# Kernel tuning notes

Hardware: AMD Instinct MI355X
Metric: run time of the kernel (lower is better)

The kernel has to match this reference:

```python
import jax, jax.numpy as jnp
import numpy as np

TAU = 0.5

def setup_inputs() -> dict:
    key = jax.random.key(0)
    kx, ky = jax.random.split(key)
    B, H = 8192, 256
    x = jax.random.normal(kx, (B, H), dtype=jnp.float32)
    y = jax.random.normal(ky, (B, H), dtype=jnp.float32)
    return {"x": x, "y": y}

def reference(x, y):
    # L2-normalize rows
    x_norm = x / jnp.linalg.norm(x, axis=1, keepdims=True)
    y_norm = y / jnp.linalg.norm(y, axis=1, keepdims=True)
    xy_norm = jnp.concatenate([x_norm, y_norm], axis=0)  # [2N, H]
    yx_norm = jnp.concatenate([y_norm, x_norm], axis=0)  # [2N, H]
    # [2N, 2N] cosine-similarity matrix (dominant memory traffic)
    sim_mat_1 = xy_norm @ xy_norm.T
    exp_mat = jnp.exp(sim_mat_1 / TAU)
    exp_row_sum = jnp.sum(exp_mat, axis=1)
    exp_diag = jnp.diagonal(exp_mat)
    denominator = exp_row_sum - exp_diag
    # diag(xy_norm @ yx_norm.T) is the row-wise dot product (avoids redundant NxN matmul)
    pos_sim = jnp.sum(xy_norm * yx_norm, axis=1)
    numerator = jnp.exp(pos_sim / TAU)
    nt_xent = -jnp.log(numerator / denominator)
    return jnp.mean(nt_xent)
```

## Files before the change

### kernel.cpp

```cpp
#include <hip/hip_runtime.h>
#include <hip/hip_bf16.h>
#include <hip/hip_fp8.h>
#include <math.h>

constexpr int NROWS = 8192;
constexpr int HDIM  = 256;
constexpr int N2    = 16384;
constexpr int BM    = 128;
constexpr int NTILE = N2 / BM;
constexpr int NBLK  = NTILE * (NTILE + 1) / 2;

constexpr float ZSCALE    = 16.0f;
constexpr float ACC2EXP2  = 2.885390082f / 256.0f;

typedef __attribute__((ext_vector_type(4))) float floatx4;

#define DPP_ADD(v, CTRL) do {                                                \
    union { float f; int i; } _u, _r; _u.f = (v);                            \
    _r.i = __builtin_amdgcn_update_dpp(0, _u.i, (CTRL), 0xF, 0xF, true);     \
    (v) += _r.f; } while (0)
#define DPP_ROW_SUM16(v) do { DPP_ADD(v,0x101); DPP_ADD(v,0x102);            \
    DPP_ADD(v,0x104); DPP_ADD(v,0x108); } while (0)
#define DPP_ALL_SUM16(v) do { DPP_ADD(v,0xB1); DPP_ADD(v,0x4E);              \
    DPP_ADD(v,0x124); DPP_ADD(v,0x128); } while (0)


__global__ __launch_bounds__(256) void normalize_kernel(
    const float* __restrict__ x, const float* __restrict__ y,
    unsigned char* __restrict__ Zp8, float* __restrict__ pos,
    float* __restrict__ rowsum, float* __restrict__ out)
{
    const int wave = threadIdx.x >> 6, lane = threadIdx.x & 63;
    const int row  = blockIdx.x * 4 + wave;

    const float4 xv = ((const float4*)x)[row * 64 + lane];
    const float4 yv = ((const float4*)y)[row * 64 + lane];

    float sx  = xv.x*xv.x + xv.y*xv.y + xv.z*xv.z + xv.w*xv.w;
    float sy  = yv.x*yv.x + yv.y*yv.y + yv.z*yv.z + yv.w*yv.w;
    float sxy = xv.x*yv.x + xv.y*yv.y + xv.z*yv.z + xv.w*yv.w;
    DPP_ALL_SUM16(sx); DPP_ALL_SUM16(sy); DPP_ALL_SUM16(sxy);
    sx  += __shfl_xor(sx, 16);  sx  += __shfl_xor(sx, 32);
    sy  += __shfl_xor(sy, 16);  sy  += __shfl_xor(sy, 32);
    sxy += __shfl_xor(sxy, 16); sxy += __shfl_xor(sxy, 32);

    const float rxn = rsqrtf(sx), ryn = rsqrtf(sy);
    const float rx = rxn * ZSCALE, ry = ryn * ZSCALE;

    auto pack4 = [](float a, float b, float c, float d) -> unsigned int {
        __hip_fp8_e4m3 f0(a), f1(b), f2(c), f3(d);
        return (unsigned int)f0.__x | ((unsigned int)f1.__x << 8) |
               ((unsigned int)f2.__x << 16) | ((unsigned int)f3.__x << 24);
    };
    const unsigned int wx = pack4(xv.x * rx, xv.y * rx, xv.z * rx, xv.w * rx);
    const unsigned int wy = pack4(yv.x * ry, yv.y * ry, yv.z * ry, yv.w * ry);

    const int tile = row >> 4, m = row & 15;
    const size_t off = (size_t)tile * 4096 + (lane >> 1) * 128 + m * 8 + (lane & 1) * 4;
    *(unsigned int*)(Zp8 + off)                         = wx;
    *(unsigned int*)(Zp8 + off + (size_t)512 * 4096)    = wy;

    if (lane == 0) {
        const float p = sxy * rxn * ryn;
        pos[row]         = p;
        pos[row + NROWS] = p;
    }
    const int gt = blockIdx.x * 256 + threadIdx.x;
    if (gt < N2) rowsum[gt] = 0.f;
    if (gt == 0) out[0] = 0.f;
}

__global__ __launch_bounds__(256, 4) void simgemm_kernel(
    const unsigned char* __restrict__ Zp8, float* __restrict__ rowsum)
{
    const int b = blockIdx.x;
    const int k = b & 7;
    const int m = b >> 3;
    int bi, bj;
    if (m < 136) {
        int ti = (int)((33.0f - sqrtf(1089.0f - 8.0f * (float)m)) * 0.5f);
        if (m < ti * (33 - ti) / 2) ti--;
        else if (m >= (ti + 1) * (32 - ti) / 2) ti++;
        const int tj = ti + (m - ti * (33 - ti) / 2);
        bi = k * 16 + ti;
        bj = k * 16 + tj;
    } else {
        const int m2 = m - 136;
        const int hh = m2 >> 7;
        const int r  = m2 & 127;
        const int h  = hh * 8 + k;
        const int q  = h >> 1;
        const int sub = h & 1;
        int gi = 0;
        #pragma unroll
        for (int t = 6; t > 0; --t)
            if (q >= t * (15 - t) / 2) { gi = t; break; }
        const int gj = gi + 1 + (q - gi * (15 - gi) / 2);
        bi = gi * 16 + sub * 8 + (r >> 4);
        bj = gj * 16 + (r & 15);
    }
    const bool diag = (bi == bj);

    __shared__ float rs[BM];
    __shared__ float cs[BM];

    const int tid  = threadIdx.x;
    const int wave = tid >> 6;
    const int lane = tid & 63;
    const int wm   = wave & 1;
    const int wn   = wave >> 1;
    const int g    = lane >> 4;
    const int m15  = lane & 15;

    if (tid < BM) { rs[tid] = 0.f; cs[tid] = 0.f; }
    __syncthreads();

    const unsigned char* pA = Zp8 + (size_t)(bi * 8 + wm * 4) * 4096 + lane * 8;
    const unsigned char* pB = Zp8 + (size_t)(bj * 8 + wn * 4) * 4096 + lane * 8;

    floatx4 acc[4][4] = {};
    long af[3][4], bf[3][4];

    #pragma unroll
    for (int f = 0; f < 4; ++f) {
        af[0][f] = *(const long*)(pA + f * 4096);
        bf[0][f] = *(const long*)(pB + f * 4096);
    }
    #pragma unroll
    for (int f = 0; f < 4; ++f) {
        af[1][f] = *(const long*)(pA + f * 4096 + 512);
        bf[1][f] = *(const long*)(pB + f * 4096 + 512);
    }

    #pragma unroll
    for (int s = 0; s < HDIM / 32; ++s) {
        const int cur = s % 3;
        if (s + 2 < HDIM / 32) {
            const int nxt = (s + 2) % 3;
            #pragma unroll
            for (int f = 0; f < 4; ++f) {
                af[nxt][f] = *(const long*)(pA + f * 4096 + (s + 2) * 512);
                bf[nxt][f] = *(const long*)(pB + f * 4096 + (s + 2) * 512);
            }
        }
        #pragma unroll
        for (int fm = 0; fm < 4; ++fm)
            #pragma unroll
            for (int fn = 0; fn < 4; ++fn)
                acc[fm][fn] = __builtin_amdgcn_mfma_f32_16x16x32_fp8_fp8(
                    af[cur][fm], bf[cur][fn], acc[fm][fn], 0, 0, 0);
    }

    float rp[4][4] = {{0.f}};
    float cp[4]    = {0.f};

    if (!diag) {
        #pragma unroll
        for (int fm = 0; fm < 4; ++fm)
            #pragma unroll
            for (int fn = 0; fn < 4; ++fn) {
                const floatx4 a = acc[fm][fn];
                #pragma unroll
                for (int q = 0; q < 4; ++q) {
                    const float e = __builtin_amdgcn_exp2f(a[q] * ACC2EXP2);
                    rp[fm][q] += e;
                    cp[fn]    += e;
                }
            }
    } else {
        #pragma unroll
        for (int fm = 0; fm < 4; ++fm)
            #pragma unroll
            for (int fn = 0; fn < 4; ++fn) {
                const floatx4 a = acc[fm][fn];
                const int cl = wn * 64 + fn * 16 + m15;
                #pragma unroll
                for (int q = 0; q < 4; ++q) {
                    const int rl = wm * 64 + fm * 16 + g * 4 + q;
                    float e = __builtin_amdgcn_exp2f(a[q] * ACC2EXP2);
                    if (cl <= rl) e = 0.f;
                    rp[fm][q] += e;
                    cp[fn]    += e;
                }
            }
    }

    #pragma unroll
    for (int fm = 0; fm < 4; ++fm)
        #pragma unroll
        for (int q = 0; q < 4; ++q) {
            float v = rp[fm][q];
            DPP_ROW_SUM16(v);
            rp[fm][q] = v;
        }
    if (m15 == 0) {
        #pragma unroll
        for (int fm = 0; fm < 4; ++fm)
            #pragma unroll
            for (int q = 0; q < 4; ++q)
                atomicAdd(&rs[wm * 64 + fm * 16 + g * 4 + q], rp[fm][q]);
    }

    #pragma unroll
    for (int mask = 16; mask < 64; mask <<= 1)
        #pragma unroll
        for (int fn = 0; fn < 4; ++fn)
            cp[fn] += __shfl_xor(cp[fn], mask);
    if (g == 0) {
        #pragma unroll
        for (int fn = 0; fn < 4; ++fn)
            atomicAdd(&cs[wn * 64 + fn * 16 + m15], cp[fn]);
    }

    __syncthreads();
    if (tid < BM) {
        atomicAdd(&rowsum[(size_t)bi * BM + tid], rs[tid]);
        atomicAdd(&rowsum[(size_t)bj * BM + tid], cs[tid]);
    }
}

__global__ __launch_bounds__(1024) void finalize_kernel(
    const float* __restrict__ rowsum, const float* __restrict__ pos,
    float* __restrict__ out)
{
    const int i = threadIdx.x + blockIdx.x * 1024;
    float s = logf(rowsum[i]) - 2.0f * pos[i];
    #pragma unroll
    for (int off = 32; off; off >>= 1) s += __shfl_down(s, off);
    __shared__ float sh[16];
    const int lt = threadIdx.x;
    if ((lt & 63) == 0) sh[lt >> 6] = s;
    __syncthreads();
    if (lt == 0) {
        float tot = 0.f;
        #pragma unroll
        for (int w = 0; w < 16; ++w) tot += sh[w];
        atomicAdd(out, tot / (float)N2);
    }
}

extern "C" void kernel_launch(void* const* d_in, const int* in_sizes, int n_in,
                              void* d_out, int out_size, void* d_ws, size_t ws_size,
                              hipStream_t stream)
{
    const float* x = (const float*)d_in[0];
    const float* y = (const float*)d_in[1];

    unsigned char* Zp8 = (unsigned char*)d_ws;
    float* rowsum = (float*)((char*)d_ws + (size_t)N2 * HDIM);
    float* pos    = rowsum + N2;

    normalize_kernel<<<NROWS / 4, 256, 0, stream>>>(x, y, Zp8, pos, rowsum, (float*)d_out);
    simgemm_kernel<<<NBLK, 256, 0, stream>>>(Zp8, rowsum);
    finalize_kernel<<<N2 / 1024, 1024, 0, stream>>>(rowsum, pos, (float*)d_out);
}
```

Before: 163.3 us.

## Switch to 32x32x16 FP8 MFMA layout and fuse finalize via last-block reduction

Repacks the normalized FP8 matrix into 32-row tiles and replaces the 16x16x32 MFMA with the 32x32x16 variant, reshaping the epilogue reductions for the new accumulator layout. The finalize kernel is removed: each GEMM block bumps a global counter and the last block computes the log-sum loss. The aim is fewer MFMA instructions and operand loads per tile plus one less kernel launch. The cost is a serial tail reduction in a single block and a weaker memory-ordering pattern, since the counter uses relaxed atomics.

New measurement: 194.7 us. 19.2% more time.

```diff
diff --git a/kernel.cpp b/kernel.cpp
--- a/kernel.cpp
+++ b/kernel.cpp
@@ -13,22 +13,23 @@
 constexpr float ZSCALE    = 16.0f;
 constexpr float ACC2EXP2  = 2.885390082f / 256.0f;
 
-typedef __attribute__((ext_vector_type(4))) float floatx4;
+typedef __attribute__((ext_vector_type(16))) float floatx16;
 
 #define DPP_ADD(v, CTRL) do {                                                \
     union { float f; int i; } _u, _r; _u.f = (v);                            \
     _r.i = __builtin_amdgcn_update_dpp(0, _u.i, (CTRL), 0xF, 0xF, true);     \
     (v) += _r.f; } while (0)
-#define DPP_ROW_SUM16(v) do { DPP_ADD(v,0x101); DPP_ADD(v,0x102);            \
-    DPP_ADD(v,0x104); DPP_ADD(v,0x108); } while (0)
 #define DPP_ALL_SUM16(v) do { DPP_ADD(v,0xB1); DPP_ADD(v,0x4E);              \
     DPP_ADD(v,0x124); DPP_ADD(v,0x128); } while (0)
+#define DPP_SUM32_TO_L31(v) do { DPP_ADD(v,0x111); DPP_ADD(v,0x112);         \
+    DPP_ADD(v,0x114); DPP_ADD(v,0x118); DPP_ADD(v,0x142); } while (0)
 
 
 __global__ __launch_bounds__(256) void normalize_kernel(
     const float* __restrict__ x, const float* __restrict__ y,
     unsigned char* __restrict__ Zp8, float* __restrict__ pos,
-    float* __restrict__ rowsum, float* __restrict__ out)
+    float* __restrict__ rowsum, int* __restrict__ counter,
+    float* __restrict__ out)
 {
     const int wave = threadIdx.x >> 6, lane = threadIdx.x & 63;
     const int row  = blockIdx.x * 4 + wave;
@@ -55,10 +56,10 @@
     const unsigned int wx = pack4(xv.x * rx, xv.y * rx, xv.z * rx, xv.w * rx);
     const unsigned int wy = pack4(yv.x * ry, yv.y * ry, yv.z * ry, yv.w * ry);
 
-    const int tile = row >> 4, m = row & 15;
-    const size_t off = (size_t)tile * 4096 + (lane >> 1) * 128 + m * 8 + (lane & 1) * 4;
+    const size_t off = (size_t)(row >> 5) * 8192 + (lane >> 1) * 256
+                     + (row & 31) * 8 + (lane & 1) * 4;
     *(unsigned int*)(Zp8 + off)                         = wx;
-    *(unsigned int*)(Zp8 + off + (size_t)512 * 4096)    = wy;
+    *(unsigned int*)(Zp8 + off + (size_t)256 * 8192)    = wy;
 
     if (lane == 0) {
         const float p = sxy * rxn * ryn;
@@ -67,11 +68,13 @@
     }
     const int gt = blockIdx.x * 256 + threadIdx.x;
     if (gt < N2) rowsum[gt] = 0.f;
-    if (gt == 0) out[0] = 0.f;
+    if (gt == 0) { *counter = 0; out[0] = 0.f; }
 }
 
 __global__ __launch_bounds__(256, 4) void simgemm_kernel(
-    const unsigned char* __restrict__ Zp8, float* __restrict__ rowsum)
+    const unsigned char* __restrict__ Zp8, float* __restrict__ rowsum,
+    const float* __restrict__ pos, int* __restrict__ counter,
+    float* __restrict__ out)
 {
     const int b = blockIdx.x;
     const int k = b & 7;
@@ -103,113 +106,100 @@
 
     __shared__ float rs[BM];
     __shared__ float cs[BM];
+    __shared__ int   isLast;
 
     const int tid  = threadIdx.x;
     const int wave = tid >> 6;
     const int lane = tid & 63;
     const int wm   = wave & 1;
     const int wn   = wave >> 1;
-    const int g    = lane >> 4;
-    const int m15  = lane & 15;
+    const int hl   = lane >> 5;
+    const int c31  = lane & 31;
 
     if (tid < BM) { rs[tid] = 0.f; cs[tid] = 0.f; }
     __syncthreads();
 
-    const unsigned char* pA = Zp8 + (size_t)(bi * 8 + wm * 4) * 4096 + lane * 8;
-    const unsigned char* pB = Zp8 + (size_t)(bj * 8 + wn * 4) * 4096 + lane * 8;
-
-    floatx4 acc[4][4] = {};
+    const unsigned char* pA = Zp8 + (size_t)(bi * 4 + wm * 2) * 8192 + lane * 8;
+    const unsigned char* pB = Zp8 + (size_t)(bj * 4 + wn * 2) * 8192 + lane * 8;
+
+    floatx16 acc[2][2] = {};
     long af[3][4], bf[3][4];
 
-    #pragma unroll
-    for (int f = 0; f < 4; ++f) {
-        af[0][f] = *(const long*)(pA + f * 4096);
-        bf[0][f] = *(const long*)(pB + f * 4096);
-    }
-    #pragma unroll
-    for (int f = 0; f < 4; ++f) {
-        af[1][f] = *(const long*)(pA + f * 4096 + 512);
-        bf[1][f] = *(const long*)(pB + f * 4096 + 512);
-    }
-
-    #pragma unroll
-    for (int s = 0; s < HDIM / 32; ++s) {
+    auto loadm = [&](int buf, int s2) {
+        af[buf][0] = *(const long*)(pA + (s2 * 2 + 0) * 512);
+        af[buf][1] = *(const long*)(pA + (s2 * 2 + 1) * 512);
+        af[buf][2] = *(const long*)(pA + 8192 + (s2 * 2 + 0) * 512);
+        af[buf][3] = *(const long*)(pA + 8192 + (s2 * 2 + 1) * 512);
+        bf[buf][0] = *(const long*)(pB + (s2 * 2 + 0) * 512);
+        bf[buf][1] = *(const long*)(pB + (s2 * 2 + 1) * 512);
+        bf[buf][2] = *(const long*)(pB + 8192 + (s2 * 2 + 0) * 512);
+        bf[buf][3] = *(const long*)(pB + 8192 + (s2 * 2 + 1) * 512);
+    };
+
+    loadm(0, 0);
+    loadm(1, 1);
+
+    #pragma unroll
+    for (int s = 0; s < 8; ++s) {
         const int cur = s % 3;
-        if (s + 2 < HDIM / 32) {
-            const int nxt = (s + 2) % 3;
+        if (s + 2 < 8) loadm((s + 2) % 3, s + 2);
+        #pragma unroll
+        for (int u = 0; u < 2; ++u)
             #pragma unroll
-            for (int f = 0; f < 4; ++f) {
-                af[nxt][f] = *(const long*)(pA + f * 4096 + (s + 2) * 512);
-                bf[nxt][f] = *(const long*)(pB + f * 4096 + (s + 2) * 512);
+            for (int fm = 0; fm < 2; ++fm)
+                #pragma unroll
+                for (int fn = 0; fn < 2; ++fn)
+                    acc[fm][fn] = __builtin_amdgcn_mfma_f32_32x32x16_fp8_fp8(
+                        af[cur][fm * 2 + u], bf[cur][fn * 2 + u],
+                        acc[fm][fn], 0, 0, 0);
+    }
+
+    float rp[2][16];
+    float cp[2] = {0.f, 0.f};
+    #pragma unroll
+    for (int fm = 0; fm < 2; ++fm)
+        #pragma unroll
+        for (int reg = 0; reg < 16; ++reg) rp[fm][reg] = 0.f;
+
+    #pragma unroll
+    for (int fm = 0; fm < 2; ++fm)
+        #pragma unroll
+        for (int fn = 0; fn < 2; ++fn) {
+            const floatx16 a = acc[fm][fn];
+            #pragma unroll
+            for (int reg = 0; reg < 16; ++reg) {
+                float e = __builtin_amdgcn_exp2f(a[reg] * ACC2EXP2);
+                if (diag) {
+                    const int rl = wm * 64 + fm * 32 + (reg & 3) + 8 * (reg >> 2) + 4 * hl;
+                    const int cl = wn * 64 + fn * 32 + c31;
+                    if (cl <= rl) e = 0.f;
+                }
+                rp[fm][reg] += e;
+                cp[fn]      += e;
             }
         }
-        #pragma unroll
-        for (int fm = 0; fm < 4; ++fm)
+
+    #pragma unroll
+    for (int fm = 0; fm < 2; ++fm)
+        #pragma unroll
+        for (int reg = 0; reg < 16; ++reg) {
+            float v = rp[fm][reg];
+            DPP_SUM32_TO_L31(v);
+            rp[fm][reg] = v;
+        }
+    if (c31 == 31) {
+        #pragma unroll
+        for (int fm = 0; fm < 2; ++fm)
             #pragma unroll
-            for (int fn = 0; fn < 4; ++fn)
-                acc[fm][fn] = __builtin_amdgcn_mfma_f32_16x16x32_fp8_fp8(
-                    af[cur][fm], bf[cur][fn], acc[fm][fn], 0, 0, 0);
-    }
-
-    float rp[4][4] = {{0.f}};
-    float cp[4]    = {0.f};
-
-    if (!diag) {
-        #pragma unroll
-        for (int fm = 0; fm < 4; ++fm)
-            #pragma unroll
-            for (int fn = 0; fn < 4; ++fn) {
-                const floatx4 a = acc[fm][fn];
-                #pragma unroll
-                for (int q = 0; q < 4; ++q) {
-                    const float e = __builtin_amdgcn_exp2f(a[q] * ACC2EXP2);
-                    rp[fm][q] += e;
-                    cp[fn]    += e;
-                }
-            }
-    } else {
-        #pragma unroll
-        for (int fm = 0; fm < 4; ++fm)
-            #pragma unroll
-            for (int fn = 0; fn < 4; ++fn) {
-                const floatx4 a = acc[fm][fn];
-                const int cl = wn * 64 + fn * 16 + m15;
-                #pragma unroll
-                for (int q = 0; q < 4; ++q) {
-                    const int rl = wm * 64 + fm * 16 + g * 4 + q;
-                    float e = __builtin_amdgcn_exp2f(a[q] * ACC2EXP2);
-                    if (cl <= rl) e = 0.f;
-                    rp[fm][q] += e;
-                    cp[fn]    += e;
-                }
-            }
-    }
-
-    #pragma unroll
-    for (int fm = 0; fm < 4; ++fm)
-        #pragma unroll
-        for (int q = 0; q < 4; ++q) {
-            float v = rp[fm][q];
-            DPP_ROW_SUM16(v);
-            rp[fm][q] = v;
-        }
-    if (m15 == 0) {
-        #pragma unroll
-        for (int fm = 0; fm < 4; ++fm)
-            #pragma unroll
-            for (int q = 0; q < 4; ++q)
-                atomicAdd(&rs[wm * 64 + fm * 16 + g * 4 + q], rp[fm][q]);
-    }
-
-    #pragma unroll
-    for (int mask = 16; mask < 64; mask <<= 1)
-        #pragma unroll
-        for (int fn = 0; fn < 4; ++fn)
-            cp[fn] += __shfl_xor(cp[fn], mask);
-    if (g == 0) {
-        #pragma unroll
-        for (int fn = 0; fn < 4; ++fn)
-            atomicAdd(&cs[wn * 64 + fn * 16 + m15], cp[fn]);
+            for (int reg = 0; reg < 16; ++reg)
+                atomicAdd(&rs[wm * 64 + fm * 32 + (reg & 3) + 8 * (reg >> 2) + 4 * hl],
+                          rp[fm][reg]);
+    }
+
+    #pragma unroll
+    for (int fn = 0; fn < 2; ++fn) {
+        cp[fn] += __shfl_xor(cp[fn], 32);
+        if (hl == 0) atomicAdd(&cs[wn * 64 + fn * 32 + c31], cp[fn]);
     }
 
     __syncthreads();
@@ -217,26 +207,29 @@
         atomicAdd(&rowsum[(size_t)bi * BM + tid], rs[tid]);
         atomicAdd(&rowsum[(size_t)bj * BM + tid], cs[tid]);
     }
-}
-
-__global__ __launch_bounds__(1024) void finalize_kernel(
-    const float* __restrict__ rowsum, const float* __restrict__ pos,
-    float* __restrict__ out)
-{
-    const int i = threadIdx.x + blockIdx.x * 1024;
-    float s = logf(rowsum[i]) - 2.0f * pos[i];
-    #pragma unroll
-    for (int off = 32; off; off >>= 1) s += __shfl_down(s, off);
-    __shared__ float sh[16];
-    const int lt = threadIdx.x;
-    if ((lt & 63) == 0) sh[lt >> 6] = s;
-    __syncthreads();
-    if (lt == 0) {
-        float tot = 0.f;
-        #pragma unroll
-        for (int w = 0; w < 16; ++w) tot += sh[w];
-        atomicAdd(out, tot / (float)N2);
-    }
+
+    __syncthreads();
+    if (tid == 0) {
+        const int t = __hip_atomic_fetch_add(counter, 1, __ATOMIC_RELAXED,
+                                             __HIP_MEMORY_SCOPE_AGENT);
+        isLast = (t == NBLK - 1);
+    }
+    __syncthreads();
+    if (!isLast) return;
+
+    float s = 0.f;
+    for (int i = tid; i < N2; i += 256) {
+        const float r = __hip_atomic_fetch_add(&rowsum[i], 0.0f,
+                                               __ATOMIC_RELAXED,
+                                               __HIP_MEMORY_SCOPE_AGENT);
+        s += __logf(r) - 2.0f * pos[i];
+    }
+    #pragma unroll
+    for (int mm = 1; mm < 64; mm <<= 1) s += __shfl_xor(s, mm);
+    if (lane == 0) rs[wave] = s;
+    __syncthreads();
+    if (tid == 0)
+        out[0] = (rs[0] + rs[1] + rs[2] + rs[3]) / (float)N2;
 }
 
 extern "C" void kernel_launch(void* const* d_in, const int* in_sizes, int n_in,
@@ -247,10 +240,12 @@
     const float* y = (const float*)d_in[1];
 
     unsigned char* Zp8 = (unsigned char*)d_ws;
-    float* rowsum = (float*)((char*)d_ws + (size_t)N2 * HDIM);
-    float* pos    = rowsum + N2;
-
-    normalize_kernel<<<NROWS / 4, 256, 0, stream>>>(x, y, Zp8, pos, rowsum, (float*)d_out);
-    simgemm_kernel<<<NBLK, 256, 0, stream>>>(Zp8, rowsum);
-    finalize_kernel<<<N2 / 1024, 1024, 0, stream>>>(rowsum, pos, (float*)d_out);
+    float* rowsum  = (float*)((char*)d_ws + (size_t)N2 * HDIM);
+    float* pos     = rowsum + N2;
+    int*   counter = (int*)(pos + N2);
+
+    normalize_kernel<<<NROWS / 4, 256, 0, stream>>>(x, y, Zp8, pos, rowsum,
+                                                    counter, (float*)d_out);
+    simgemm_kernel<<<NBLK, 256, 0, stream>>>(Zp8, rowsum, pos, counter,
+                                             (float*)d_out);
 }
```
